# Kernel optimization log

Measured on AMD Instinct MI355X. Metric: run time of the kernel, lower is better.

The kernel has to match this reference:

```python
import jax, jax.numpy as jnp
import numpy as np

B, S, E, H = 4, 2048, 1024, 16
D = E // H
SCALE = np.sqrt(D).astype(np.float32)


def setup_inputs() -> dict:
    key = jax.random.key(0)
    ks = jax.random.split(key, 9)
    s = 1.0 / np.sqrt(E)
    return {
        "x": jax.random.normal(ks[0], (B, S, E), dtype=jnp.float32),
        "Wq": jax.random.uniform(ks[1], (E, E), jnp.float32, -s, s),
        "bq": jax.random.uniform(ks[2], (E,), jnp.float32, -s, s),
        "Wk": jax.random.uniform(ks[3], (E, E), jnp.float32, -s, s),
        "bk": jax.random.uniform(ks[4], (E,), jnp.float32, -s, s),
        "Wv": jax.random.uniform(ks[5], (E, E), jnp.float32, -s, s),
        "bv": jax.random.uniform(ks[6], (E,), jnp.float32, -s, s),
        "Wo": jax.random.uniform(ks[7], (E, E), jnp.float32, -s, s),
        "bo": jax.random.uniform(ks[8], (E,), jnp.float32, -s, s),
    }


def reference(x, Wq, bq, Wk, bk, Wv, bv, Wo, bo):
    # Linear projections (torch Linear: y = x @ W.T + b)
    q = x @ Wq.T + bq  # [B,S,E]
    k = x @ Wk.T + bk
    v = x @ Wv.T + bv
    # split heads -> [B,H,S,D]
    q = q.reshape(B, S, H, D).transpose(0, 2, 1, 3)
    k = k.reshape(B, S, H, D).transpose(0, 2, 1, 3)
    v = v.reshape(B, S, H, D).transpose(0, 2, 1, 3)
    scores = jnp.einsum("bhqd,bhkd->bhqk", q, k) / SCALE  # [B,H,S,S]
    attn = jax.nn.softmax(scores, axis=-1)  # dropout is identity at inference
    out = jnp.einsum("bhqk,bhkd->bhqd", attn, v)  # [B,H,S,D]
    out = out.transpose(0, 2, 1, 3).reshape(B, S, E)
    return out @ Wo.T + bo
```

## Files before the change

kernel.cpp:

```cpp
#include <hip/hip_runtime.h>
#include <math.h>

#define Bb 4
#define Ss 2048
#define Ee 1024
#define Hh 16
#define Dd 64

static constexpr int Mtot = Bb * Ss;
static constexpr size_t NK = (size_t)Ee * Ee;

typedef __bf16 bf16x8 __attribute__((ext_vector_type(8)));
typedef float  f32x16 __attribute__((ext_vector_type(16)));
typedef unsigned int uint32x2 __attribute__((ext_vector_type(2)));

extern "C" __device__ float __ocml_native_exp2_f32(float);

__device__ __forceinline__ unsigned short rne1(float x) {
  unsigned u = __float_as_uint(x);
  return (unsigned short)((u + 0x7FFFu + ((u >> 16) & 1u)) >> 16);
}
__device__ __forceinline__ short4 rne4(const float4 v) {
  short4 r;
  r.x = (short)rne1(v.x); r.y = (short)rne1(v.y);
  r.z = (short)rne1(v.z); r.w = (short)rne1(v.w);
  return r;
}

__global__ __launch_bounds__(256) void prep(const float* __restrict__ x,
                                            const float* __restrict__ wq,
                                            const float* __restrict__ wk,
                                            const float* __restrict__ wv,
                                            const float* __restrict__ wo,
                                            unsigned short* __restrict__ xb,
                                            unsigned short* __restrict__ wqkv,
                                            unsigned short* __restrict__ wob) {
  const int X4 = (int)((size_t)Mtot * Ee / 4);
  const int W4 = (int)(NK / 4);
  const int i = blockIdx.x * 256 + threadIdx.x;
  const float* src;
  unsigned short* dst;
  int off;
  if (i < X4) {
    src = x; dst = xb; off = i;
  } else {
    const int j = i - X4;
    const int seg = j >> 18;
    off = j & (W4 - 1);
    if (seg == 0)      { src = wq; dst = wqkv; }
    else if (seg == 1) { src = wk; dst = wqkv + NK; }
    else if (seg == 2) { src = wv; dst = wqkv + 2 * NK; }
    else               { src = wo; dst = wob; }
  }
  float4 v = ((const float4*)src)[off];
  ((short4*)dst)[off] = rne4(v);
}

__device__ __forceinline__ void gemm_core(const unsigned short* __restrict__ A,
                                          const unsigned short* __restrict__ W,
                                          unsigned short* sm, int bm, int bn,
                                          int tid, f32x16 acc[2][2]) {
  unsigned short* sA = sm;
  unsigned short* sW = sm + 9216;
  const int r  = tid >> 1;
  const int ch = (tid & 1) << 5;
  const int lane = tid & 63, w = tid >> 6;
  const int wm = (w & 1) << 6, wn = (w >> 1) << 6;
  const int m32 = lane & 31, g = lane >> 5;

  const unsigned short* A0 = A + (size_t)(bm + r) * Ee + ch;
  const unsigned short* W0 = W + (size_t)(bn + r) * Ee + ch;
  const int so = r * 72 + ch;

  uint4 a0 = *(const uint4*)(A0);
  uint4 a1 = *(const uint4*)(A0 + 8);
  uint4 a2 = *(const uint4*)(A0 + 16);
  uint4 a3 = *(const uint4*)(A0 + 24);
  uint4 w0 = *(const uint4*)(W0);
  uint4 w1 = *(const uint4*)(W0 + 8);
  uint4 w2 = *(const uint4*)(W0 + 16);
  uint4 w3 = *(const uint4*)(W0 + 24);

  for (int k0 = 0; k0 < Ee; k0 += 64) {
    __syncthreads();
    *(uint4*)(sA + so)      = a0; *(uint4*)(sA + so + 8)  = a1;
    *(uint4*)(sA + so + 16) = a2; *(uint4*)(sA + so + 24) = a3;
    *(uint4*)(sW + so)      = w0; *(uint4*)(sW + so + 8)  = w1;
    *(uint4*)(sW + so + 16) = w2; *(uint4*)(sW + so + 24) = w3;
    __syncthreads();
    if (k0 + 64 < Ee) {
      const unsigned short* An = A0 + k0 + 64;
      const unsigned short* Wn = W0 + k0 + 64;
      a0 = *(const uint4*)(An);
      a1 = *(const uint4*)(An + 8);
      a2 = *(const uint4*)(An + 16);
      a3 = *(const uint4*)(An + 24);
      w0 = *(const uint4*)(Wn);
      w1 = *(const uint4*)(Wn + 8);
      w2 = *(const uint4*)(Wn + 16);
      w3 = *(const uint4*)(Wn + 24);
    }
#pragma unroll
    for (int kk = 0; kk < 64; kk += 16) {
      const int kc = kk + (g << 3);
      bf16x8 af[2], wf[2];
#pragma unroll
      for (int s = 0; s < 2; ++s) {
        af[s] = *(const bf16x8*)(sA + (wm + (s << 5) + m32) * 72 + kc);
        wf[s] = *(const bf16x8*)(sW + (wn + (s << 5) + m32) * 72 + kc);
      }
#pragma unroll
      for (int si = 0; si < 2; ++si)
#pragma unroll
        for (int sj = 0; sj < 2; ++sj)
          acc[si][sj] = __builtin_amdgcn_mfma_f32_32x32x16_bf16(af[si], wf[sj], acc[si][sj], 0, 0, 0);
    }
  }
}


__global__ __launch_bounds__(256) void gemm_qkv(const unsigned short* __restrict__ xb,
                                                const unsigned short* __restrict__ wqkv,
                                                const float* __restrict__ bq,
                                                const float* __restrict__ bk,
                                                const float* __restrict__ bv,
                                                unsigned short* __restrict__ Qb,
                                                unsigned short* __restrict__ Kb,
                                                unsigned short* __restrict__ Vt) {
  __shared__ unsigned short sm[18432];
  f32x16 acc[2][2] = {};
  const int tid = threadIdx.x;
  const int bm = blockIdx.x << 7, bn = blockIdx.y << 7;
  gemm_core(xb, wqkv, sm, bm, bn, tid, acc);

  const int lane = tid & 63, w = tid >> 6;
  const int wm = (w & 1) << 6, wn = (w >> 1) << 6;
  const int m32 = lane & 31, g = lane >> 5;
  const int proj = blockIdx.y >> 3;
  const int cb   = (blockIdx.y & 7) << 7;
  const float* bp = proj == 0 ? bq : (proj == 1 ? bk : bv);
  const float SC = 0.18033688011112042f;

  if (proj == 2) {
    const int bmS = bm & (Ss - 1);
    const int b = bm >> 11;
#pragma unroll
    for (int si = 0; si < 2; ++si)
#pragma unroll
      for (int sj = 0; sj < 2; ++sj) {
        const int col = cb + wn + (sj << 5) + m32;
        const int hh = col >> 6, dd = col & 63;
        const float bvv = bp[col];
        unsigned short* vrow = Vt + ((size_t)((b * Hh + hh) * Dd + dd)) * Ss;
#pragma unroll
        for (int rq = 0; rq < 4; ++rq) {
          const int s0 = bmS + wm + (si << 5) + (g << 2) + (rq << 3);
          float4 v;
          v.x = acc[si][sj][rq * 4 + 0] + bvv;
          v.y = acc[si][sj][rq * 4 + 1] + bvv;
          v.z = acc[si][sj][rq * 4 + 2] + bvv;
          v.w = acc[si][sj][rq * 4 + 3] + bvv;
          *(short4*)(vrow + s0) = rne4(v);
        }
      }
  } else {
    unsigned short* dst = proj == 0 ? Qb : Kb;
    const float sc = proj == 0 ? SC : 1.0f;
#pragma unroll
    for (int si = 0; si < 2; ++si)
#pragma unroll
      for (int sj = 0; sj < 2; ++sj) {
        const int col = cb + wn + (sj << 5) + m32;
        const int hh = col >> 6, dd = col & 63;
        const float bvv = bp[col];
#pragma unroll
        for (int reg = 0; reg < 16; ++reg) {
          const int row = bm + wm + (si << 5) + (g << 2) + (reg & 3) + ((reg >> 2) << 3);
          const int b = row >> 11, s = row & (Ss - 1);
          dst[((size_t)((b * Hh + hh) * Ss + s)) * Dd + dd] =
              rne1((acc[si][sj][reg] + bvv) * sc);
        }
      }
  }
}

__global__ __launch_bounds__(256) void gemm_out(const unsigned short* __restrict__ Ab,
                                                const unsigned short* __restrict__ Wb,
                                                const float* __restrict__ bias,
                                                float* __restrict__ C) {
  __shared__ unsigned short sm[18432];
  f32x16 acc[2][2] = {};
  const int tid = threadIdx.x;
  const int bm = blockIdx.x << 7, bn = blockIdx.y << 7;
  gemm_core(Ab, Wb, sm, bm, bn, tid, acc);
  const int lane = tid & 63, w = tid >> 6;
  const int wm = (w & 1) << 6, wn = (w >> 1) << 6;
  const int m32 = lane & 31, g = lane >> 5;
#pragma unroll
  for (int si = 0; si < 2; ++si)
#pragma unroll
    for (int sj = 0; sj < 2; ++sj) {
      const int col = bn + wn + (sj << 5) + m32;
      const float bv = bias[col];
#pragma unroll
      for (int reg = 0; reg < 16; ++reg) {
        const int row = bm + wm + (si << 5) + (g << 2) + (reg & 3) + ((reg >> 2) << 3);
        C[(size_t)row * Ee + col] = acc[si][sj][reg] + bv;
      }
    }
}

__global__ __launch_bounds__(256) void flash_mfma(const unsigned short* __restrict__ Qb,
                                                  const unsigned short* __restrict__ Kb,
                                                  const unsigned short* __restrict__ Vt,
                                                  unsigned short* __restrict__ Ob) {
  __shared__ unsigned short smem[9216];
  unsigned short* Kh = smem;
  unsigned short* Vh = smem + 4608;
  const int tid = threadIdx.x;
  const int lane = tid & 63, w = tid >> 6;
  const int m32 = lane & 31, g = lane >> 5;
  const int qt = blockIdx.x << 7;
  const int bh = blockIdx.y;

  const size_t ph = (size_t)bh * Ss * Dd;
  const unsigned short* qp = Qb + ph + (size_t)(qt + (w << 5) + m32) * Dd + (g << 3);
  bf16x8 qf[4];
#pragma unroll
  for (int c = 0; c < 4; ++c) qf[c] = *(const bf16x8*)(qp + (c << 4));

  const int sr = tid >> 2;
  const int sc = (tid & 3) << 4;
  const unsigned short* kg = Kb + ph + (size_t)sr * Dd + sc;
  const unsigned short* vg = Vt + (size_t)bh * Dd * Ss + (size_t)sr * Ss + sc;
  const int so = sr * 72 + sc;

  uint4 k0 = *(const uint4*)(kg);
  uint4 k1 = *(const uint4*)(kg + 8);
  uint4 v0 = *(const uint4*)(vg);
  uint4 v1 = *(const uint4*)(vg + 8);

  f32x16 acc_o[2] = {};
  float l_ = 0.f;

  for (int kt = 0; kt < Ss; kt += 64) {
    __syncthreads();
    *(uint4*)(&Kh[so]) = k0; *(uint4*)(&Kh[so + 8]) = k1;
    *(uint4*)(&Vh[so]) = v0; *(uint4*)(&Vh[so + 8]) = v1;
    __syncthreads();
    if (kt + 64 < Ss) {
      const unsigned short* kg2 = kg + (size_t)(kt + 64) * Dd;
      const unsigned short* vg2 = vg + (kt + 64);
      k0 = *(const uint4*)(kg2);
      k1 = *(const uint4*)(kg2 + 8);
      v0 = *(const uint4*)(vg2);
      v1 = *(const uint4*)(vg2 + 8);
    }

    float p[2][16];
#pragma unroll
    for (int mt = 0; mt < 2; ++mt) {
      f32x16 a = {};
#pragma unroll
      for (int c = 0; c < 4; ++c) {
        bf16x8 kf = *(const bf16x8*)(&Kh[((mt << 5) + m32) * 72 + (c << 4) + (g << 3)]);
        a = __builtin_amdgcn_mfma_f32_32x32x16_bf16(kf, qf[c], a, 0, 0, 0);
      }
#pragma unroll
      for (int r = 0; r < 16; ++r) p[mt][r] = a[r];
    }
    float rs = 0.f;
#pragma unroll
    for (int mt = 0; mt < 2; ++mt)
#pragma unroll
      for (int r = 0; r < 16; ++r) {
        float e = __ocml_native_exp2_f32(p[mt][r]);
        e = __uint_as_float(__float_as_uint(e) & 0xFFFF0000u);
        p[mt][r] = e;
        rs += e;
      }
    rs += __shfl_xor(rs, 32);
    l_ += rs;

#pragma unroll
    for (int c = 0; c < 4; ++c) {
      const int mt = c >> 1, b8 = (c & 1) << 3;
      unsigned dw0 = __builtin_amdgcn_perm(__float_as_uint(p[mt][b8 + 1]), __float_as_uint(p[mt][b8 + 0]), 0x07060302u);
      unsigned dw1 = __builtin_amdgcn_perm(__float_as_uint(p[mt][b8 + 3]), __float_as_uint(p[mt][b8 + 2]), 0x07060302u);
      unsigned dw2 = __builtin_amdgcn_perm(__float_as_uint(p[mt][b8 + 5]), __float_as_uint(p[mt][b8 + 4]), 0x07060302u);
      unsigned dw3 = __builtin_amdgcn_perm(__float_as_uint(p[mt][b8 + 7]), __float_as_uint(p[mt][b8 + 6]), 0x07060302u);
      const uint32x2 s02 = __builtin_amdgcn_permlane32_swap(dw0, dw2, false, false);
      const uint32x2 s13 = __builtin_amdgcn_permlane32_swap(dw1, dw3, false, false);
      union { unsigned u[4]; bf16x8 v; } pf;
      pf.u[0] = s02[0];
      pf.u[1] = s13[0];
      pf.u[2] = s02[1];
      pf.u[3] = s13[1];
#pragma unroll
      for (int dt = 0; dt < 2; ++dt) {
        bf16x8 vf = *(const bf16x8*)(&Vh[((dt << 5) + m32) * 72 + (c << 4) + (g << 3)]);
        acc_o[dt] = __builtin_amdgcn_mfma_f32_32x32x16_bf16(vf, pf.v, acc_o[dt], 0, 0, 0);
      }
    }
  }

  const float inv = 1.0f / l_;
  const int q = (w << 5) + m32;
  unsigned short* Of = smem;
  __syncthreads();
#pragma unroll
  for (int dt = 0; dt < 2; ++dt)
#pragma unroll
    for (int r = 0; r < 16; ++r) {
      const int d = (dt << 5) + (g << 2) + (r & 3) + ((r >> 2) << 3);
      Of[q * 72 + d] = rne1(acc_o[dt][r] * inv);
    }
  __syncthreads();
  const int orow = tid >> 1, oc = (tid & 1) << 5;
  const int bq = bh >> 4, hh = bh & 15;
  const size_t obase = ((size_t)(bq * Ss + qt + orow)) * Ee + hh * Dd + oc;
#pragma unroll
  for (int i = 0; i < 2; ++i)
    *(uint4*)(Ob + obase + (i << 3)) = *(const uint4*)(&Of[orow * 72 + oc + (i << 3)]);
#pragma unroll
  for (int i = 2; i < 4; ++i)
    *(uint4*)(Ob + obase + (i << 3)) = *(const uint4*)(&Of[orow * 72 + oc + (i << 3)]);
}

extern "C" void kernel_launch(void* const* d_in, const int* in_sizes, int n_in,
                              void* d_out, int out_size, void* d_ws, size_t ws_size,
                              hipStream_t stream) {
  const float* x  = (const float*)d_in[0];
  const float* Wq = (const float*)d_in[1];
  const float* bq = (const float*)d_in[2];
  const float* Wk = (const float*)d_in[3];
  const float* bk = (const float*)d_in[4];
  const float* Wv = (const float*)d_in[5];
  const float* bv = (const float*)d_in[6];
  const float* Wo = (const float*)d_in[7];
  const float* bo = (const float*)d_in[8];
  float* out = (float*)d_out;

  const size_t nX = (size_t)Mtot * Ee;
  unsigned short* xb   = (unsigned short*)d_ws;
  unsigned short* qb   = xb + nX;
  unsigned short* kb   = qb + nX;
  unsigned short* vt   = kb + nX;
  unsigned short* ob   = vt + nX;
  unsigned short* wqkv = ob + nX;
  unsigned short* wob  = wqkv + 3 * NK;

  const int total4 = (int)(nX / 4 + NK);
  prep<<<total4 / 256, 256, 0, stream>>>(x, Wq, Wk, Wv, Wo, xb, wqkv, wob);

  gemm_qkv<<<dim3(Mtot / 128, 3 * Ee / 128), 256, 0, stream>>>(xb, wqkv, bq, bk, bv, qb, kb, vt);

  flash_mfma<<<dim3(Ss / 128, Bb * Hh), 256, 0, stream>>>(qb, kb, vt, ob);

  gemm_out<<<dim3(Mtot / 128, Ee / 128), 256, 0, stream>>>(ob, wob, bo, out);
}
```

Baseline: 299.6 us.

## Load GEMM tiles directly into LDS with XOR-swizzled layout

The GEMM core now uses global_load_lds to move A and W tiles straight from global memory into shared memory, bypassing registers. It replaces the padded 72-wide rows with 64-wide rows and an XOR swizzle to avoid bank conflicts, which shrinks the LDS footprint. The old register-prefetch of the next k-tile is removed, so global loads are no longer overlapped with the MFMA work of the previous tile. Each iteration now waits on the direct loads at the barrier, which risks exposing memory latency.

```diff
diff --git a/kernel.cpp b/kernel.cpp
--- a/kernel.cpp
+++ b/kernel.cpp
@@ -15,6 +15,9 @@
 typedef unsigned int uint32x2 __attribute__((ext_vector_type(2)));
 
 extern "C" __device__ float __ocml_native_exp2_f32(float);
+
+#define AS1(p) ((const __attribute__((address_space(1))) void*)(p))
+#define AS3(p) ((__attribute__((address_space(3))) void*)(p))
 
 __device__ __forceinline__ unsigned short rne1(float x) {
   unsigned u = __float_as_uint(x);
@@ -61,53 +64,37 @@
                                           unsigned short* sm, int bm, int bn,
                                           int tid, f32x16 acc[2][2]) {
   unsigned short* sA = sm;
-  unsigned short* sW = sm + 9216;
-  const int r  = tid >> 1;
-  const int ch = (tid & 1) << 5;
+  unsigned short* sW = sm + 8192;
   const int lane = tid & 63, w = tid >> 6;
   const int wm = (w & 1) << 6, wn = (w >> 1) << 6;
   const int m32 = lane & 31, g = lane >> 5;
-
-  const unsigned short* A0 = A + (size_t)(bm + r) * Ee + ch;
-  const unsigned short* W0 = W + (size_t)(bn + r) * Ee + ch;
-  const int so = r * 72 + ch;
-
-  uint4 a0 = *(const uint4*)(A0);
-  uint4 a1 = *(const uint4*)(A0 + 8);
-  uint4 a2 = *(const uint4*)(A0 + 16);
-  uint4 a3 = *(const uint4*)(A0 + 24);
-  uint4 w0 = *(const uint4*)(W0);
-  uint4 w1 = *(const uint4*)(W0 + 8);
-  uint4 w2 = *(const uint4*)(W0 + 16);
-  uint4 w3 = *(const uint4*)(W0 + 24);
+  const int sw = m32 & 7;
+
+  const int srow = (w << 5) + (lane >> 3);
+  const int scol = ((lane & 7) ^ (lane >> 3)) << 3;
+  const unsigned short* Ag = A + (size_t)(bm + srow) * Ee + scol;
+  const unsigned short* Wg = W + (size_t)(bn + srow) * Ee + scol;
+  unsigned short* sAw = sA + (w << 11);
+  unsigned short* sWw = sW + (w << 11);
 
   for (int k0 = 0; k0 < Ee; k0 += 64) {
     __syncthreads();
-    *(uint4*)(sA + so)      = a0; *(uint4*)(sA + so + 8)  = a1;
-    *(uint4*)(sA + so + 16) = a2; *(uint4*)(sA + so + 24) = a3;
-    *(uint4*)(sW + so)      = w0; *(uint4*)(sW + so + 8)  = w1;
-    *(uint4*)(sW + so + 16) = w2; *(uint4*)(sW + so + 24) = w3;
+#pragma unroll
+    for (int i = 0; i < 4; ++i) {
+      __builtin_amdgcn_global_load_lds(AS1(Ag + (size_t)(i << 3) * Ee + k0),
+                                       AS3(sAw + (i << 9)), 16, 0, 0);
+      __builtin_amdgcn_global_load_lds(AS1(Wg + (size_t)(i << 3) * Ee + k0),
+                                       AS3(sWw + (i << 9)), 16, 0, 0);
+    }
     __syncthreads();
-    if (k0 + 64 < Ee) {
-      const unsigned short* An = A0 + k0 + 64;
-      const unsigned short* Wn = W0 + k0 + 64;
-      a0 = *(const uint4*)(An);
-      a1 = *(const uint4*)(An + 8);
-      a2 = *(const uint4*)(An + 16);
-      a3 = *(const uint4*)(An + 24);
-      w0 = *(const uint4*)(Wn);
-      w1 = *(const uint4*)(Wn + 8);
-      w2 = *(const uint4*)(Wn + 16);
-      w3 = *(const uint4*)(Wn + 24);
-    }
 #pragma unroll
     for (int kk = 0; kk < 64; kk += 16) {
-      const int kc = kk + (g << 3);
+      const int ch = (((kk >> 3) | g) ^ sw) << 3;
       bf16x8 af[2], wf[2];
 #pragma unroll
       for (int s = 0; s < 2; ++s) {
-        af[s] = *(const bf16x8*)(sA + (wm + (s << 5) + m32) * 72 + kc);
-        wf[s] = *(const bf16x8*)(sW + (wn + (s << 5) + m32) * 72 + kc);
+        af[s] = *(const bf16x8*)(sA + ((wm + (s << 5) + m32) << 6) + ch);
+        wf[s] = *(const bf16x8*)(sW + ((wn + (s << 5) + m32) << 6) + ch);
       }
 #pragma unroll
       for (int si = 0; si < 2; ++si)
@@ -127,7 +114,7 @@
                                                 unsigned short* __restrict__ Qb,
                                                 unsigned short* __restrict__ Kb,
                                                 unsigned short* __restrict__ Vt) {
-  __shared__ unsigned short sm[18432];
+  __shared__ unsigned short sm[16384];
   f32x16 acc[2][2] = {};
   const int tid = threadIdx.x;
   const int bm = blockIdx.x << 7, bn = blockIdx.y << 7;
@@ -188,7 +175,7 @@
                                                 const unsigned short* __restrict__ Wb,
                                                 const float* __restrict__ bias,
                                                 float* __restrict__ C) {
-  __shared__ unsigned short sm[18432];
+  __shared__ unsigned short sm[16384];
   f32x16 acc[2][2] = {};
   const int tid = threadIdx.x;
   const int bm = blockIdx.x << 7, bn = blockIdx.y << 7;
```

After: 292.9 us. -2.2%, faster.
